# Kernel optimization log

Hardware: AMD Instinct MI355X
Metric: run time of the kernel (lower is better)

Reference implementation:

```python
import jax, jax.numpy as jnp
import numpy as np


def setup_inputs() -> dict:
    key = jax.random.key(0)
    ks = jax.random.split(key, 9)
    B, C, PF = 4, 256, 4096
    C8 = C // 8
    scale_qk = 1.0 / np.sqrt(C)
    return {
        "x": jax.random.normal(ks[0], (B, C, PF), dtype=jnp.float32),
        "xh1": jax.random.normal(ks[1], (B, C, PF), dtype=jnp.float32),
        "xl1": jax.random.normal(ks[2], (B, C, PF), dtype=jnp.float32),
        "Wq": jax.random.normal(ks[3], (C8, C), dtype=jnp.float32) * scale_qk,
        "bq": jnp.zeros((C8,), dtype=jnp.float32),
        "Wk": jax.random.normal(ks[4], (C8, C), dtype=jnp.float32) * scale_qk,
        "bk": jnp.zeros((C8,), dtype=jnp.float32),
        "Wv": jax.random.normal(ks[5], (C, C), dtype=jnp.float32) * scale_qk,
        "bv": jnp.zeros((C,), dtype=jnp.float32),
        "gamma1": jnp.array([0.5], dtype=jnp.float32),
        "gamma2": jnp.array([0.5], dtype=jnp.float32),
    }


def reference(x, xh1, xl1, Wq, bq, Wk, bk, Wv, bv, gamma1, gamma2):
    # x, xh1, xl1: (B, C, N) with N = H*W. Conv1x1 == channel-wise linear,
    # so the (B,C,H,W) reshape in the original is a no-op for the math.
    q = jnp.einsum("oc,bcn->bon", Wq, x) + bq[None, :, None]   # (B, C/8, N)
    k = jnp.einsum("oc,bcn->bon", Wk, x) + bk[None, :, None]   # (B, C/8, N)
    # energy[b, n, m] = q[:, :, n] . k[:, :, m]  (NO 1/sqrt(d) scale, as in source)
    energy = jnp.einsum("bcn,bcm->bnm", q, k)                  # (B, N, N)
    attention = jax.nn.softmax(energy, axis=-1)                # softmax over keys m
    vh = jnp.einsum("oc,bcn->bon", Wv, xh1) + bv[None, :, None]  # (B, C, N)
    vl = jnp.einsum("oc,bcn->bon", Wv, xl1) + bv[None, :, None]  # (B, C, N)
    # out = V @ attention^T : out[b, c, n] = sum_m vh[b, c, m] * attention[b, n, m]
    outh = jnp.einsum("bcm,bnm->bcn", vh, attention)
    outl = jnp.einsum("bcm,bnm->bcn", vl, attention)
    outh = xh1 * (gamma1 * outh)
    outl = xl1 * (gamma2 * outl)
    return outh, outl
```

## Files before the change

### kernel.cpp

```cpp
#include <hip/hip_runtime.h>
#include <math.h>

#define B_  4
#define C_  256
#define C8_ 32
#define N_  4096

typedef __attribute__((ext_vector_type(8))) short          bf16x8;
typedef __attribute__((ext_vector_type(8))) unsigned short us8;
typedef __attribute__((ext_vector_type(4))) float          f32x4;
typedef __attribute__((ext_vector_type(2))) float          f32x2;

__device__ inline unsigned short f2bf(float f) {
    unsigned u = __float_as_uint(f);
    u += 0x7FFFu + ((u >> 16) & 1u);
    return (unsigned short)(u >> 16);
}
__device__ inline unsigned pack2bf(float a, float b) {
    return (unsigned)f2bf(a) | ((unsigned)f2bf(b) << 16);
}

__global__ __launch_bounds__(256) void qk_proj_k(
    const float* __restrict__ x,  const float* __restrict__ Wq,
    const float* __restrict__ bq, const float* __restrict__ Wk,
    const float* __restrict__ bk, float* __restrict__ qt,
    float* __restrict__ ktt)
{
    __shared__ float Ws[64][36];
    __shared__ float Xs[32][132];
    const int b  = blockIdx.y;
    const int m0 = blockIdx.x * 128;
    const int t  = threadIdx.x;
    const int tx = t & 15;
    const int ty = t >> 4;
    const float* xb = x + (size_t)b * C_ * N_;

    float acc[4][8];
    #pragma unroll
    for (int i = 0; i < 4; ++i)
        #pragma unroll
        for (int j = 0; j < 8; ++j) acc[i][j] = 0.f;

    for (int k0 = 0; k0 < C_; k0 += 32) {
        __syncthreads();
        #pragma unroll
        for (int i = 0; i < 2; ++i) {
            int idx = t + i * 256, cc = idx >> 3, j = idx & 7;
            const float* src = (cc < 32 ? Wq + cc * C_ : Wk + (cc - 32) * C_) + k0 + j * 4;
            *(f32x4*)&Ws[cc][j * 4] = *(const f32x4*)src;
        }
        #pragma unroll
        for (int i = 0; i < 4; ++i) {
            int idx = t + i * 256, k = idx >> 5, j = idx & 31;
            *(f32x4*)&Xs[k][j * 4] = *(const f32x4*)(xb + (size_t)(k0 + k) * N_ + m0 + j * 4);
        }
        __syncthreads();
        for (int k = 0; k < 32; ++k) {
            float wv[4];
            #pragma unroll
            for (int i = 0; i < 4; ++i) wv[i] = Ws[ty * 4 + i][k];
            f32x4 x0 = *(const f32x4*)&Xs[k][tx * 8];
            f32x4 x1 = *(const f32x4*)&Xs[k][tx * 8 + 4];
            #pragma unroll
            for (int i = 0; i < 4; ++i) {
                acc[i][0] = fmaf(wv[i], x0[0], acc[i][0]);
                acc[i][1] = fmaf(wv[i], x0[1], acc[i][1]);
                acc[i][2] = fmaf(wv[i], x0[2], acc[i][2]);
                acc[i][3] = fmaf(wv[i], x0[3], acc[i][3]);
                acc[i][4] = fmaf(wv[i], x1[0], acc[i][4]);
                acc[i][5] = fmaf(wv[i], x1[1], acc[i][5]);
                acc[i][6] = fmaf(wv[i], x1[2], acc[i][6]);
                acc[i][7] = fmaf(wv[i], x1[3], acc[i][7]);
            }
        }
    }
    #pragma unroll
    for (int i = 0; i < 4; ++i) {
        const int cl = ty * 4 + i;
        if (cl < 32) {
            const float bqq = bq[cl];
            #pragma unroll
            for (int j = 0; j < 8; ++j)
                qt[((size_t)b * N_ + m0 + tx * 8 + j) * C8_ + cl] = acc[i][j] + bqq;
        } else {
            const float bkk = bk[cl - 32];
            f32x4 o0, o1;
            #pragma unroll
            for (int j = 0; j < 4; ++j) { o0[j] = acc[i][j] + bkk; o1[j] = acc[i][j + 4] + bkk; }
            float* dst = ktt + ((size_t)b * C8_ + cl - 32) * N_ + m0 + tx * 8;
            *(f32x4*)dst = o0;
            *(f32x4*)(dst + 4) = o1;
        }
    }
}

__global__ __launch_bounds__(256) void v_proj_k(
    const float* __restrict__ xh1, const float* __restrict__ xl1,
    const float* __restrict__ Wv,  const float* __restrict__ bv,
    unsigned short* __restrict__ vtc)
{
    __shared__ float Ws[64][36];
    __shared__ float Xs[32][132];
    const int b   = blockIdx.z & 3;
    const int s   = blockIdx.z >> 2;
    const int cc0 = blockIdx.y * 64;
    const int m0  = blockIdx.x * 128;
    const int t   = threadIdx.x;
    const int tx  = t & 15;
    const int ty  = t >> 4;
    const float* xb = (s ? xl1 : xh1) + (size_t)b * C_ * N_;

    float acc[4][8];
    #pragma unroll
    for (int i = 0; i < 4; ++i)
        #pragma unroll
        for (int j = 0; j < 8; ++j) acc[i][j] = 0.f;

    for (int k0 = 0; k0 < C_; k0 += 32) {
        __syncthreads();
        #pragma unroll
        for (int i = 0; i < 2; ++i) {
            int idx = t + i * 256, cc = idx >> 3, j = idx & 7;
            *(f32x4*)&Ws[cc][j * 4] = *(const f32x4*)(Wv + (size_t)(cc0 + cc) * C_ + k0 + j * 4);
        }
        #pragma unroll
        for (int i = 0; i < 4; ++i) {
            int idx = t + i * 256, k = idx >> 5, j = idx & 31;
            *(f32x4*)&Xs[k][j * 4] = *(const f32x4*)(xb + (size_t)(k0 + k) * N_ + m0 + j * 4);
        }
        __syncthreads();
        for (int k = 0; k < 32; ++k) {
            float wv[4];
            #pragma unroll
            for (int i = 0; i < 4; ++i) wv[i] = Ws[ty * 4 + i][k];
            f32x4 x0 = *(const f32x4*)&Xs[k][tx * 8];
            f32x4 x1 = *(const f32x4*)&Xs[k][tx * 8 + 4];
            #pragma unroll
            for (int i = 0; i < 4; ++i) {
                acc[i][0] = fmaf(wv[i], x0[0], acc[i][0]);
                acc[i][1] = fmaf(wv[i], x0[1], acc[i][1]);
                acc[i][2] = fmaf(wv[i], x0[2], acc[i][2]);
                acc[i][3] = fmaf(wv[i], x0[3], acc[i][3]);
                acc[i][4] = fmaf(wv[i], x1[0], acc[i][4]);
                acc[i][5] = fmaf(wv[i], x1[1], acc[i][5]);
                acc[i][6] = fmaf(wv[i], x1[2], acc[i][6]);
                acc[i][7] = fmaf(wv[i], x1[3], acc[i][7]);
            }
        }
    }
    #pragma unroll
    for (int i = 0; i < 4; ++i) {
        const int cc = cc0 + ty * 4 + i;
        const float bvv = bv[cc];
        us8 w;
        #pragma unroll
        for (int j = 0; j < 8; ++j) w[j] = f2bf(acc[i][j] + bvv);
        *(us8*)&vtc[((size_t)b * 512 + s * 256 + cc) * N_ + m0 + tx * 8] = w;
    }
}

__global__ __launch_bounds__(512, 4) void pv_k(
    const float* __restrict__ qt, const float* __restrict__ ktt,
    const unsigned short* __restrict__ vtc,
    const float* __restrict__ xh1, const float* __restrict__ xl1,
    const float* __restrict__ g1, const float* __restrict__ g2,
    float* __restrict__ out)
{
    __shared__ float          Kst[2][32][36];
    __shared__ unsigned short Ps[32][32];
    __shared__ unsigned short Vs[2][512][32];
    __shared__ float          Zrow[32];

    const int id   = blockIdx.x;
    const int b    = (id >> 1) & 3;
    const int nblk = ((id >> 3) << 1) | (id & 1);
    const int n0   = nblk * 32;

    const int t    = threadIdx.x;
    const int w    = t >> 6, lane = t & 63;
    const int lr   = lane & 15, ls = lane >> 4;
    const int wn   = w * 64;
    const int er   = t >> 4;
    const int eg   = t & 15;

    float q[32];
    {
        const float* qrow = qt + ((size_t)b * N_ + n0 + er) * C8_;
        #pragma unroll
        for (int c4 = 0; c4 < 8; ++c4) {
            f32x4 v = *(const f32x4*)(qrow + c4 * 4);
            q[c4*4+0] = v[0]; q[c4*4+1] = v[1]; q[c4*4+2] = v[2]; q[c4*4+3] = v[3];
        }
    }

    f32x4 acc[2][4];
    #pragma unroll
    for (int i = 0; i < 2; ++i)
        #pragma unroll
        for (int j = 0; j < 4; ++j) acc[i][j] = (f32x4){0.f, 0.f, 0.f, 0.f};
    float zpart = 0.f;

    const float*          kb   = ktt + (size_t)b * C8_ * N_;
    const unsigned short* vcol = vtc + (size_t)b * 512 * N_ + (size_t)t * N_;
    const int   kc   = t >> 3, kj = t & 7;
    const float* kptr = kb + (size_t)kc * N_ + kj * 4;
    const int   vsw  = (t >> 1) & 3;

    us8   vreg[4];
    f32x4 kreg;

    #pragma unroll
    for (int i = 0; i < 4; ++i) vreg[i] = *(const us8*)(vcol + i * 8);
    if (t < 256) kreg = *(const f32x4*)(kptr);
    #pragma unroll
    for (int i = 0; i < 4; ++i) *(us8*)&Vs[0][t][(i ^ vsw) * 8] = vreg[i];
    if (t < 256) *(f32x4*)&Kst[0][kc][kj * 4] = kreg;
    #pragma unroll
    for (int i = 0; i < 4; ++i) vreg[i] = *(const us8*)(vcol + 32 + i * 8);
    if (t < 256) kreg = *(const f32x4*)(kptr + 32);
    __syncthreads();

    int p = 0;
    for (int tile = 0; tile < N_ / 32; ++tile) {
        if (tile + 1 < N_ / 32) {
            #pragma unroll
            for (int i = 0; i < 4; ++i) *(us8*)&Vs[p ^ 1][t][(i ^ vsw) * 8] = vreg[i];
            if (t < 256) *(f32x4*)&Kst[p ^ 1][kc][kj * 4] = kreg;
        }
        if (tile + 2 < N_ / 32) {
            const int moff = (tile + 2) * 32;
            #pragma unroll
            for (int i = 0; i < 4; ++i) vreg[i] = *(const us8*)(vcol + moff + i * 8);
            if (t < 256) kreg = *(const f32x4*)(kptr + moff);
        }
        {
            float e0 = 0.f, e1 = 0.f;
            #pragma unroll
            for (int c = 0; c < 32; ++c) {
                f32x2 kv = *(const f32x2*)&Kst[p][c][eg * 2];
                e0 = fmaf(q[c], kv[0], e0);
                e1 = fmaf(q[c], kv[1], e1);
            }
            float p0 = __expf(e0 - 20.f);
            float p1 = __expf(e1 - 20.f);
            zpart += p0 + p1;
            *(unsigned*)&Ps[er][eg * 2] = pack2bf(p0, p1);
        }
        __syncthreads();
        {
            bf16x8 a0 = *(const bf16x8*)&Ps[lr][ls * 8];
            bf16x8 a1 = *(const bf16x8*)&Ps[16 + lr][ls * 8];
            #pragma unroll
            for (int fj = 0; fj < 4; ++fj) {
                const int col  = wn + fj * 16 + lr;
                const int slot = ls ^ ((col >> 1) & 3);
                bf16x8 bfr = *(const bf16x8*)&Vs[p][col][slot * 8];
                acc[0][fj] = __builtin_amdgcn_mfma_f32_16x16x32_bf16(a0, bfr, acc[0][fj], 0, 0, 0);
                acc[1][fj] = __builtin_amdgcn_mfma_f32_16x16x32_bf16(a1, bfr, acc[1][fj], 0, 0, 0);
            }
        }
        __syncthreads();
        p ^= 1;
    }

    #pragma unroll
    for (int m = 1; m < 16; m <<= 1) zpart += __shfl_xor(zpart, m, 16);
    if (eg == 0) Zrow[er] = zpart;
    __syncthreads();

    float rzf[2][4];
    #pragma unroll
    for (int fi = 0; fi < 2; ++fi)
        #pragma unroll
        for (int r = 0; r < 4; ++r) rzf[fi][r] = 1.f / Zrow[fi * 16 + ls * 4 + r];

    const float g1v = g1[0], g2v = g2[0];
    #pragma unroll
    for (int fi = 0; fi < 2; ++fi) {
        const int nb = fi * 16 + ls * 4;
        #pragma unroll
        for (int fj = 0; fj < 4; ++fj) {
            const int cc = wn + fj * 16 + lr;
            const int st = cc >> 8;
            const float  gv = st ? g2v : g1v;
            const float* xg = st ? xl1 : xh1;
            float* og = out + (st ? (size_t)B_ * C_ * N_ : (size_t)0);
            const size_t base = ((size_t)b * C_ + (cc & 255)) * N_ + n0 + nb;
            f32x4 xv = *(const f32x4*)(xg + base);
            f32x4 o;
            #pragma unroll
            for (int r = 0; r < 4; ++r)
                o[r] = xv[r] * (gv * (acc[fi][fj][r] * rzf[fi][r]));
            *(f32x4*)(og + base) = o;
        }
    }
}

extern "C" void kernel_launch(void* const* d_in, const int* in_sizes, int n_in,
                              void* d_out, int out_size, void* d_ws, size_t ws_size,
                              hipStream_t stream)
{
    const float* x   = (const float*)d_in[0];
    const float* xh1 = (const float*)d_in[1];
    const float* xl1 = (const float*)d_in[2];
    const float* Wq  = (const float*)d_in[3];
    const float* bq  = (const float*)d_in[4];
    const float* Wk  = (const float*)d_in[5];
    const float* bk  = (const float*)d_in[6];
    const float* Wv  = (const float*)d_in[7];
    const float* bv  = (const float*)d_in[8];
    const float* g1  = (const float*)d_in[9];
    const float* g2  = (const float*)d_in[10];
    float* out = (float*)d_out;

    char* pws = (char*)d_ws;
    float* qt  = (float*)pws;                 pws += (size_t)B_ * N_ * C8_ * 4;
    float* ktt = (float*)pws;                 pws += (size_t)B_ * N_ * C8_ * 4;
    unsigned short* vtc = (unsigned short*)pws;

    qk_proj_k<<<dim3(N_ / 128, B_),      256, 0, stream>>>(x, Wq, bq, Wk, bk, qt, ktt);
    v_proj_k <<<dim3(N_ / 128, 4, B_*2), 256, 0, stream>>>(xh1, xl1, Wv, bv, vtc);
    pv_k     <<<dim3((N_ / 32) * B_),    512, 0, stream>>>(qt, ktt, vtc,
                                                           xh1, xl1, g1, g2, out);
}
```

Before: 464.5 us.

## Use split-bf16 MFMA for projections and QK energy, stream V from registers

Replaces the FP32 FMA projection kernels with one templated kernel that splits inputs and weights into bf16 high/low parts and runs three MFMAs per product to approximate FP32 accuracy. In the attention kernel the scalar QK dot products move to split-bf16 MFMAs on half the waves while the other half stage K, and V fragments now load straight from global memory into registers, dropping the shared-memory V buffer. It also remaps blocks to group work by batch. This trades scalar FMA throughput for matrix-core throughput, at the cost of conversion overhead and a small precision loss.

```diff
diff --git a/kernel.cpp b/kernel.cpp
--- a/kernel.cpp
+++ b/kernel.cpp
@@ -5,157 +5,136 @@
 #define C_  256
 #define C8_ 32
 #define N_  4096
+#define NT_ 128
 
 typedef __attribute__((ext_vector_type(8))) short          bf16x8;
 typedef __attribute__((ext_vector_type(8))) unsigned short us8;
+typedef __attribute__((ext_vector_type(4))) unsigned short us4;
 typedef __attribute__((ext_vector_type(4))) float          f32x4;
-typedef __attribute__((ext_vector_type(2))) float          f32x2;
 
 __device__ inline unsigned short f2bf(float f) {
     unsigned u = __float_as_uint(f);
     u += 0x7FFFu + ((u >> 16) & 1u);
     return (unsigned short)(u >> 16);
 }
-__device__ inline unsigned pack2bf(float a, float b) {
-    return (unsigned)f2bf(a) | ((unsigned)f2bf(b) << 16);
-}
-
-__global__ __launch_bounds__(256) void qk_proj_k(
-    const float* __restrict__ x,  const float* __restrict__ Wq,
-    const float* __restrict__ bq, const float* __restrict__ Wk,
-    const float* __restrict__ bk, float* __restrict__ qt,
-    float* __restrict__ ktt)
+__device__ inline void splitbf(float v, unsigned short& h, unsigned short& l) {
+    unsigned short hh = f2bf(v);
+    float hf = __uint_as_float((unsigned)hh << 16);
+    h = hh; l = f2bf(v - hf);
+}
+__device__ inline bf16x8 asb(us8 v) { return __builtin_bit_cast(bf16x8, v); }
+
+template<int MODE>
+__global__ __launch_bounds__(256, 4) void proj_k(
+    const float* __restrict__ Xa, const float* __restrict__ Xb,
+    const float* __restrict__ Wa, const float* __restrict__ Wb,
+    const float* __restrict__ ba, const float* __restrict__ bb,
+    float* __restrict__ qt, float* __restrict__ ktt,
+    unsigned short* __restrict__ vtc)
 {
-    __shared__ float Ws[64][36];
-    __shared__ float Xs[32][132];
-    const int b  = blockIdx.y;
-    const int m0 = blockIdx.x * 128;
-    const int t  = threadIdx.x;
-    const int tx = t & 15;
-    const int ty = t >> 4;
-    const float* xb = x + (size_t)b * C_ * N_;
-
-    float acc[4][8];
+    __shared__ unsigned short XsH[32][66], XsL[32][66];
+    __shared__ unsigned short WsH[64][40], WsL[64][40];
+
+    const int m0 = blockIdx.x * 64;
+    int b, s, cc0;
+    const float* xptr;
+    if (MODE == 0) { b = blockIdx.z; s = 0; cc0 = 0;
+                     xptr = Xa + (size_t)b * C_ * N_; }
+    else           { b = blockIdx.z & 3; s = blockIdx.z >> 2; cc0 = blockIdx.y * 64;
+                     xptr = (s ? Xb : Xa) + (size_t)b * C_ * N_; }
+
+    const int t = threadIdx.x;
+    const int w = t >> 6, lane = t & 63, lr = lane & 15, ls = lane >> 4;
+
+    f32x4 acc[4];
     #pragma unroll
-    for (int i = 0; i < 4; ++i)
-        #pragma unroll
-        for (int j = 0; j < 8; ++j) acc[i][j] = 0.f;
+    for (int i = 0; i < 4; ++i) acc[i] = (f32x4){0.f, 0.f, 0.f, 0.f};
+
+    const int skk = t >> 3, smo = (t & 7) * 8;
+    const int scc = t >> 2, sko = (t & 3) * 8;
+    const float* wrow;
+    if (MODE == 0) wrow = (scc < 32) ? (Wa + (size_t)scc * C_) : (Wb + (size_t)(scc - 32) * C_);
+    else           wrow = Wa + (size_t)(cc0 + scc) * C_;
 
     for (int k0 = 0; k0 < C_; k0 += 32) {
         __syncthreads();
-        #pragma unroll
-        for (int i = 0; i < 2; ++i) {
-            int idx = t + i * 256, cc = idx >> 3, j = idx & 7;
-            const float* src = (cc < 32 ? Wq + cc * C_ : Wk + (cc - 32) * C_) + k0 + j * 4;
-            *(f32x4*)&Ws[cc][j * 4] = *(const f32x4*)src;
-        }
-        #pragma unroll
-        for (int i = 0; i < 4; ++i) {
-            int idx = t + i * 256, k = idx >> 5, j = idx & 31;
-            *(f32x4*)&Xs[k][j * 4] = *(const f32x4*)(xb + (size_t)(k0 + k) * N_ + m0 + j * 4);
+        {
+            const float* src = xptr + (size_t)(k0 + skk) * N_ + m0 + smo;
+            f32x4 a = *(const f32x4*)src, c = *(const f32x4*)(src + 4);
+            unsigned short h[8], l[8];
+            splitbf(a[0],h[0],l[0]); splitbf(a[1],h[1],l[1]);
+            splitbf(a[2],h[2],l[2]); splitbf(a[3],h[3],l[3]);
+            splitbf(c[0],h[4],l[4]); splitbf(c[1],h[5],l[5]);
+            splitbf(c[2],h[6],l[6]); splitbf(c[3],h[7],l[7]);
+            unsigned* dh = (unsigned*)&XsH[skk][smo];
+            unsigned* dl = (unsigned*)&XsL[skk][smo];
+            #pragma unroll
+            for (int i = 0; i < 4; ++i) {
+                dh[i] = (unsigned)h[2*i] | ((unsigned)h[2*i+1] << 16);
+                dl[i] = (unsigned)l[2*i] | ((unsigned)l[2*i+1] << 16);
+            }
+        }
+        {
+            f32x4 a = *(const f32x4*)(wrow + k0 + sko);
+            f32x4 c = *(const f32x4*)(wrow + k0 + sko + 4);
+            us8 h, l; unsigned short hh, ll;
+            splitbf(a[0],hh,ll); h[0]=hh; l[0]=ll;
+            splitbf(a[1],hh,ll); h[1]=hh; l[1]=ll;
+            splitbf(a[2],hh,ll); h[2]=hh; l[2]=ll;
+            splitbf(a[3],hh,ll); h[3]=hh; l[3]=ll;
+            splitbf(c[0],hh,ll); h[4]=hh; l[4]=ll;
+            splitbf(c[1],hh,ll); h[5]=hh; l[5]=ll;
+            splitbf(c[2],hh,ll); h[6]=hh; l[6]=ll;
+            splitbf(c[3],hh,ll); h[7]=hh; l[7]=ll;
+            *(us8*)&WsH[scc][sko] = h;
+            *(us8*)&WsL[scc][sko] = l;
         }
         __syncthreads();
-        for (int k = 0; k < 32; ++k) {
-            float wv[4];
-            #pragma unroll
-            for (int i = 0; i < 4; ++i) wv[i] = Ws[ty * 4 + i][k];
-            f32x4 x0 = *(const f32x4*)&Xs[k][tx * 8];
-            f32x4 x1 = *(const f32x4*)&Xs[k][tx * 8 + 4];
-            #pragma unroll
-            for (int i = 0; i < 4; ++i) {
-                acc[i][0] = fmaf(wv[i], x0[0], acc[i][0]);
-                acc[i][1] = fmaf(wv[i], x0[1], acc[i][1]);
-                acc[i][2] = fmaf(wv[i], x0[2], acc[i][2]);
-                acc[i][3] = fmaf(wv[i], x0[3], acc[i][3]);
-                acc[i][4] = fmaf(wv[i], x1[0], acc[i][4]);
-                acc[i][5] = fmaf(wv[i], x1[1], acc[i][5]);
-                acc[i][6] = fmaf(wv[i], x1[2], acc[i][6]);
-                acc[i][7] = fmaf(wv[i], x1[3], acc[i][7]);
+        us8 ahu, alu;
+        #pragma unroll
+        for (int j = 0; j < 8; ++j) {
+            ahu[j] = XsH[ls*8 + j][w*16 + lr];
+            alu[j] = XsL[ls*8 + j][w*16 + lr];
+        }
+        bf16x8 ah = asb(ahu), al = asb(alu);
+        #pragma unroll
+        for (int at = 0; at < 4; ++at) {
+            bf16x8 bh = asb(*(const us8*)&WsH[at*16 + lr][ls*8]);
+            bf16x8 bl = asb(*(const us8*)&WsL[at*16 + lr][ls*8]);
+            acc[at] = __builtin_amdgcn_mfma_f32_16x16x32_bf16(ah, bh, acc[at], 0, 0, 0);
+            acc[at] = __builtin_amdgcn_mfma_f32_16x16x32_bf16(ah, bl, acc[at], 0, 0, 0);
+            acc[at] = __builtin_amdgcn_mfma_f32_16x16x32_bf16(al, bh, acc[at], 0, 0, 0);
+        }
+    }
+
+    const int mrow = m0 + w*16 + ls*4;
+    if (MODE == 0) {
+        #pragma unroll
+        for (int at = 0; at < 4; ++at) {
+            const int cc = at*16 + lr;
+            if (at < 2) {
+                const float bia = ba[cc];
+                #pragma unroll
+                for (int r = 0; r < 4; ++r)
+                    qt[((size_t)b * N_ + mrow + r) * C8_ + cc] = acc[at][r] + bia;
+            } else {
+                const float bia = bb[cc - 32];
+                f32x4 o;
+                #pragma unroll
+                for (int r = 0; r < 4; ++r) o[r] = acc[at][r] + bia;
+                *(f32x4*)&ktt[((size_t)b * C8_ + cc - 32) * N_ + mrow] = o;
             }
         }
-    }
-    #pragma unroll
-    for (int i = 0; i < 4; ++i) {
-        const int cl = ty * 4 + i;
-        if (cl < 32) {
-            const float bqq = bq[cl];
-            #pragma unroll
-            for (int j = 0; j < 8; ++j)
-                qt[((size_t)b * N_ + m0 + tx * 8 + j) * C8_ + cl] = acc[i][j] + bqq;
-        } else {
-            const float bkk = bk[cl - 32];
-            f32x4 o0, o1;
-            #pragma unroll
-            for (int j = 0; j < 4; ++j) { o0[j] = acc[i][j] + bkk; o1[j] = acc[i][j + 4] + bkk; }
-            float* dst = ktt + ((size_t)b * C8_ + cl - 32) * N_ + m0 + tx * 8;
-            *(f32x4*)dst = o0;
-            *(f32x4*)(dst + 4) = o1;
-        }
-    }
-}
-
-__global__ __launch_bounds__(256) void v_proj_k(
-    const float* __restrict__ xh1, const float* __restrict__ xl1,
-    const float* __restrict__ Wv,  const float* __restrict__ bv,
-    unsigned short* __restrict__ vtc)
-{
-    __shared__ float Ws[64][36];
-    __shared__ float Xs[32][132];
-    const int b   = blockIdx.z & 3;
-    const int s   = blockIdx.z >> 2;
-    const int cc0 = blockIdx.y * 64;
-    const int m0  = blockIdx.x * 128;
-    const int t   = threadIdx.x;
-    const int tx  = t & 15;
-    const int ty  = t >> 4;
-    const float* xb = (s ? xl1 : xh1) + (size_t)b * C_ * N_;
-
-    float acc[4][8];
-    #pragma unroll
-    for (int i = 0; i < 4; ++i)
-        #pragma unroll
-        for (int j = 0; j < 8; ++j) acc[i][j] = 0.f;
-
-    for (int k0 = 0; k0 < C_; k0 += 32) {
-        __syncthreads();
-        #pragma unroll
-        for (int i = 0; i < 2; ++i) {
-            int idx = t + i * 256, cc = idx >> 3, j = idx & 7;
-            *(f32x4*)&Ws[cc][j * 4] = *(const f32x4*)(Wv + (size_t)(cc0 + cc) * C_ + k0 + j * 4);
-        }
-        #pragma unroll
-        for (int i = 0; i < 4; ++i) {
-            int idx = t + i * 256, k = idx >> 5, j = idx & 31;
-            *(f32x4*)&Xs[k][j * 4] = *(const f32x4*)(xb + (size_t)(k0 + k) * N_ + m0 + j * 4);
-        }
-        __syncthreads();
-        for (int k = 0; k < 32; ++k) {
-            float wv[4];
-            #pragma unroll
-            for (int i = 0; i < 4; ++i) wv[i] = Ws[ty * 4 + i][k];
-            f32x4 x0 = *(const f32x4*)&Xs[k][tx * 8];
-            f32x4 x1 = *(const f32x4*)&Xs[k][tx * 8 + 4];
-            #pragma unroll
-            for (int i = 0; i < 4; ++i) {
-                acc[i][0] = fmaf(wv[i], x0[0], acc[i][0]);
-                acc[i][1] = fmaf(wv[i], x0[1], acc[i][1]);
-                acc[i][2] = fmaf(wv[i], x0[2], acc[i][2]);
-                acc[i][3] = fmaf(wv[i], x0[3], acc[i][3]);
-                acc[i][4] = fmaf(wv[i], x1[0], acc[i][4]);
-                acc[i][5] = fmaf(wv[i], x1[1], acc[i][5]);
-                acc[i][6] = fmaf(wv[i], x1[2], acc[i][6]);
-                acc[i][7] = fmaf(wv[i], x1[3], acc[i][7]);
-            }
-        }
-    }
-    #pragma unroll
-    for (int i = 0; i < 4; ++i) {
-        const int cc = cc0 + ty * 4 + i;
-        const float bvv = bv[cc];
-        us8 w;
-        #pragma unroll
-        for (int j = 0; j < 8; ++j) w[j] = f2bf(acc[i][j] + bvv);
-        *(us8*)&vtc[((size_t)b * 512 + s * 256 + cc) * N_ + m0 + tx * 8] = w;
+    } else {
+        #pragma unroll
+        for (int at = 0; at < 4; ++at) {
+            const int cc = cc0 + at*16 + lr;
+            const float bia = ba[cc];
+            us4 o;
+            #pragma unroll
+            for (int r = 0; r < 4; ++r) o[r] = f2bf(acc[at][r] + bia);
+            *(us4*)&vtc[((size_t)b * 512 + s * 256 + cc) * N_ + mrow] = o;
+        }
     }
 }
 
@@ -166,31 +145,36 @@
     const float* __restrict__ g1, const float* __restrict__ g2,
     float* __restrict__ out)
 {
-    __shared__ float          Kst[2][32][36];
-    __shared__ unsigned short Ps[32][32];
-    __shared__ unsigned short Vs[2][512][32];
-    __shared__ float          Zrow[32];
-
-    const int id   = blockIdx.x;
-    const int b    = (id >> 1) & 3;
-    const int nblk = ((id >> 3) << 1) | (id & 1);
-    const int n0   = nblk * 32;
-
-    const int t    = threadIdx.x;
-    const int w    = t >> 6, lane = t & 63;
-    const int lr   = lane & 15, ls = lane >> 4;
-    const int wn   = w * 64;
-    const int er   = t >> 4;
-    const int eg   = t & 15;
-
-    float q[32];
-    {
-        const float* qrow = qt + ((size_t)b * N_ + n0 + er) * C8_;
-        #pragma unroll
-        for (int c4 = 0; c4 < 8; ++c4) {
-            f32x4 v = *(const f32x4*)(qrow + c4 * 4);
-            q[c4*4+0] = v[0]; q[c4*4+1] = v[1]; q[c4*4+2] = v[2]; q[c4*4+3] = v[3];
-        }
+    __shared__ unsigned short KsH[2][32][34];
+    __shared__ unsigned short KsL[2][32][34];
+    __shared__ unsigned short Ps[32][40];
+    __shared__ float          Zpart[2][32];
+
+    const int orig = blockIdx.x;
+    const int wg   = (orig & 7) * 64 + (orig >> 3);
+    const int b    = wg >> 7;
+    const int n0   = (wg & 127) * 32;
+
+    const int t = threadIdx.x, w = t >> 6, lane = t & 63;
+    const int lr = lane & 15, ls = lane >> 4;
+    const int wn = w * 64;
+    const bool ew = (w < 4);
+    const int rt = (w >> 1) & 1, mt = w & 1;
+
+    bf16x8 qh = {}, ql = {};
+    if (ew) {
+        const float* qrow = qt + ((size_t)b * N_ + n0 + rt*16 + lr) * C8_ + ls*8;
+        f32x4 q0 = *(const f32x4*)qrow, q1 = *(const f32x4*)(qrow + 4);
+        us8 hu, lu; unsigned short hh, ll;
+        splitbf(q0[0],hh,ll); hu[0]=hh; lu[0]=ll;
+        splitbf(q0[1],hh,ll); hu[1]=hh; lu[1]=ll;
+        splitbf(q0[2],hh,ll); hu[2]=hh; lu[2]=ll;
+        splitbf(q0[3],hh,ll); hu[3]=hh; lu[3]=ll;
+        splitbf(q1[0],hh,ll); hu[4]=hh; lu[4]=ll;
+        splitbf(q1[1],hh,ll); hu[5]=hh; lu[5]=ll;
+        splitbf(q1[2],hh,ll); hu[6]=hh; lu[6]=ll;
+        splitbf(q1[3],hh,ll); hu[7]=hh; lu[7]=ll;
+        qh = asb(hu); ql = asb(lu);
     }
 
     f32x4 acc[2][4];
@@ -198,89 +182,124 @@
     for (int i = 0; i < 2; ++i)
         #pragma unroll
         for (int j = 0; j < 4; ++j) acc[i][j] = (f32x4){0.f, 0.f, 0.f, 0.f};
-    float zpart = 0.f;
-
-    const float*          kb   = ktt + (size_t)b * C8_ * N_;
-    const unsigned short* vcol = vtc + (size_t)b * 512 * N_ + (size_t)t * N_;
-    const int   kc   = t >> 3, kj = t & 7;
-    const float* kptr = kb + (size_t)kc * N_ + kj * 4;
-    const int   vsw  = (t >> 1) & 3;
-
-    us8   vreg[4];
-    f32x4 kreg;
-
-    #pragma unroll
-    for (int i = 0; i < 4; ++i) vreg[i] = *(const us8*)(vcol + i * 8);
-    if (t < 256) kreg = *(const f32x4*)(kptr);
-    #pragma unroll
-    for (int i = 0; i < 4; ++i) *(us8*)&Vs[0][t][(i ^ vsw) * 8] = vreg[i];
-    if (t < 256) *(f32x4*)&Kst[0][kc][kj * 4] = kreg;
-    #pragma unroll
-    for (int i = 0; i < 4; ++i) vreg[i] = *(const us8*)(vcol + 32 + i * 8);
-    if (t < 256) kreg = *(const f32x4*)(kptr + 32);
+    float zreg[4] = {0.f, 0.f, 0.f, 0.f};
+
+    const unsigned short* vbase = vtc + (size_t)b * 512 * N_;
+    const unsigned short* vp0 = vbase + (size_t)(wn +  0 + lr) * N_ + ls*8;
+    const unsigned short* vp1 = vbase + (size_t)(wn + 16 + lr) * N_ + ls*8;
+    const unsigned short* vp2 = vbase + (size_t)(wn + 32 + lr) * N_ + ls*8;
+    const unsigned short* vp3 = vbase + (size_t)(wn + 48 + lr) * N_ + ls*8;
+
+    const int ts = t - 256, kc = (ts & 255) >> 3, kmq = (ts & 7) * 4;
+    const float* kptr = ktt + ((size_t)b * C8_ + kc) * N_ + kmq;
+
+    us8 vA0, vA1, vA2, vA3, vB0, vB1, vB2, vB3;
+
+    if (!ew) {
+        f32x4 kv = *(const f32x4*)kptr;
+        unsigned short h0,h1,h2,h3,l0,l1,l2,l3;
+        splitbf(kv[0],h0,l0); splitbf(kv[1],h1,l1);
+        splitbf(kv[2],h2,l2); splitbf(kv[3],h3,l3);
+        unsigned* dh = (unsigned*)&KsH[0][kc][kmq];
+        unsigned* dl = (unsigned*)&KsL[0][kc][kmq];
+        dh[0] = (unsigned)h0 | ((unsigned)h1 << 16);
+        dh[1] = (unsigned)h2 | ((unsigned)h3 << 16);
+        dl[0] = (unsigned)l0 | ((unsigned)l1 << 16);
+        dl[1] = (unsigned)l2 | ((unsigned)l3 << 16);
+    }
+    vA0 = *(const us8*)vp0; vA1 = *(const us8*)vp1;
+    vA2 = *(const us8*)vp2; vA3 = *(const us8*)vp3;
     __syncthreads();
 
-    int p = 0;
-    for (int tile = 0; tile < N_ / 32; ++tile) {
-        if (tile + 1 < N_ / 32) {
-            #pragma unroll
-            for (int i = 0; i < 4; ++i) *(us8*)&Vs[p ^ 1][t][(i ^ vsw) * 8] = vreg[i];
-            if (t < 256) *(f32x4*)&Kst[p ^ 1][kc][kj * 4] = kreg;
-        }
-        if (tile + 2 < N_ / 32) {
-            const int moff = (tile + 2) * 32;
-            #pragma unroll
-            for (int i = 0; i < 4; ++i) vreg[i] = *(const us8*)(vcol + moff + i * 8);
-            if (t < 256) kreg = *(const f32x4*)(kptr + moff);
-        }
-        {
-            float e0 = 0.f, e1 = 0.f;
-            #pragma unroll
-            for (int c = 0; c < 32; ++c) {
-                f32x2 kv = *(const f32x2*)&Kst[p][c][eg * 2];
-                e0 = fmaf(q[c], kv[0], e0);
-                e1 = fmaf(q[c], kv[1], e1);
+    auto body = [&](int CUR, int NXT, us8& VC0, us8& VC1, us8& VC2, us8& VC3,
+                    us8& VN0, us8& VN1, us8& VN2, us8& VN3, int TILE) {
+        const int tn = TILE + 1;
+        f32x4 kreg;
+        if (tn < NT_) {
+            VN0 = *(const us8*)(vp0 + tn*32);
+            VN1 = *(const us8*)(vp1 + tn*32);
+            VN2 = *(const us8*)(vp2 + tn*32);
+            VN3 = *(const us8*)(vp3 + tn*32);
+            if (!ew) kreg = *(const f32x4*)(kptr + tn*32);
+        }
+        if (ew) {
+            us8 khu, klu;
+            #pragma unroll
+            for (int j = 0; j < 8; ++j) {
+                khu[j] = KsH[CUR][ls*8 + j][mt*16 + lr];
+                klu[j] = KsL[CUR][ls*8 + j][mt*16 + lr];
             }
-            float p0 = __expf(e0 - 20.f);
-            float p1 = __expf(e1 - 20.f);
-            zpart += p0 + p1;
-            *(unsigned*)&Ps[er][eg * 2] = pack2bf(p0, p1);
+            bf16x8 kh = asb(khu), kl = asb(klu);
+            f32x4 ea = (f32x4){0.f, 0.f, 0.f, 0.f};
+            ea = __builtin_amdgcn_mfma_f32_16x16x32_bf16(qh, kh, ea, 0, 0, 0);
+            ea = __builtin_amdgcn_mfma_f32_16x16x32_bf16(qh, kl, ea, 0, 0, 0);
+            ea = __builtin_amdgcn_mfma_f32_16x16x32_bf16(ql, kh, ea, 0, 0, 0);
+            #pragma unroll
+            for (int r = 0; r < 4; ++r) {
+                float pe = __expf(ea[r] - 20.f);
+                zreg[r] += pe;
+                Ps[rt*16 + ls*4 + r][mt*16 + lr] = f2bf(pe);
+            }
         }
         __syncthreads();
         {
-            bf16x8 a0 = *(const bf16x8*)&Ps[lr][ls * 8];
-            bf16x8 a1 = *(const bf16x8*)&Ps[16 + lr][ls * 8];
-            #pragma unroll
-            for (int fj = 0; fj < 4; ++fj) {
-                const int col  = wn + fj * 16 + lr;
-                const int slot = ls ^ ((col >> 1) & 3);
-                bf16x8 bfr = *(const bf16x8*)&Vs[p][col][slot * 8];
-                acc[0][fj] = __builtin_amdgcn_mfma_f32_16x16x32_bf16(a0, bfr, acc[0][fj], 0, 0, 0);
-                acc[1][fj] = __builtin_amdgcn_mfma_f32_16x16x32_bf16(a1, bfr, acc[1][fj], 0, 0, 0);
-            }
+            bf16x8 pa0 = asb(*(const us8*)&Ps[lr][ls*8]);
+            bf16x8 pa1 = asb(*(const us8*)&Ps[16 + lr][ls*8]);
+            bf16x8 v0 = asb(VC0), v1 = asb(VC1), v2 = asb(VC2), v3 = asb(VC3);
+            acc[0][0] = __builtin_amdgcn_mfma_f32_16x16x32_bf16(pa0, v0, acc[0][0], 0,0,0);
+            acc[1][0] = __builtin_amdgcn_mfma_f32_16x16x32_bf16(pa1, v0, acc[1][0], 0,0,0);
+            acc[0][1] = __builtin_amdgcn_mfma_f32_16x16x32_bf16(pa0, v1, acc[0][1], 0,0,0);
+            acc[1][1] = __builtin_amdgcn_mfma_f32_16x16x32_bf16(pa1, v1, acc[1][1], 0,0,0);
+            acc[0][2] = __builtin_amdgcn_mfma_f32_16x16x32_bf16(pa0, v2, acc[0][2], 0,0,0);
+            acc[1][2] = __builtin_amdgcn_mfma_f32_16x16x32_bf16(pa1, v2, acc[1][2], 0,0,0);
+            acc[0][3] = __builtin_amdgcn_mfma_f32_16x16x32_bf16(pa0, v3, acc[0][3], 0,0,0);
+            acc[1][3] = __builtin_amdgcn_mfma_f32_16x16x32_bf16(pa1, v3, acc[1][3], 0,0,0);
+        }
+        if (tn < NT_ && !ew) {
+            unsigned short h0,h1,h2,h3,l0,l1,l2,l3;
+            splitbf(kreg[0],h0,l0); splitbf(kreg[1],h1,l1);
+            splitbf(kreg[2],h2,l2); splitbf(kreg[3],h3,l3);
+            unsigned* dh = (unsigned*)&KsH[NXT][kc][kmq];
+            unsigned* dl = (unsigned*)&KsL[NXT][kc][kmq];
+            dh[0] = (unsigned)h0 | ((unsigned)h1 << 16);
+            dh[1] = (unsigned)h2 | ((unsigned)h3 << 16);
+            dl[0] = (unsigned)l0 | ((unsigned)l1 << 16);
+            dl[1] = (unsigned)l2 | ((unsigned)l3 << 16);
         }
         __syncthreads();
-        p ^= 1;
-    }
-
-    #pragma unroll
-    for (int m = 1; m < 16; m <<= 1) zpart += __shfl_xor(zpart, m, 16);
-    if (eg == 0) Zrow[er] = zpart;
+    };
+
+    for (int tile = 0; tile < NT_; tile += 2) {
+        body(0, 1, vA0, vA1, vA2, vA3, vB0, vB1, vB2, vB3, tile);
+        body(1, 0, vB0, vB1, vB2, vB3, vA0, vA1, vA2, vA3, tile + 1);
+    }
+
+    if (ew) {
+        #pragma unroll
+        for (int r = 0; r < 4; ++r) {
+            float z = zreg[r];
+            z += __shfl_xor(z, 1, 16); z += __shfl_xor(z, 2, 16);
+            z += __shfl_xor(z, 4, 16); z += __shfl_xor(z, 8, 16);
+            if (lr == 0) Zpart[mt][rt*16 + ls*4 + r] = z;
+        }
+    }
     __syncthreads();
 
     float rzf[2][4];
     #pragma unroll
     for (int fi = 0; fi < 2; ++fi)
         #pragma unroll
-        for (int r = 0; r < 4; ++r) rzf[fi][r] = 1.f / Zrow[fi * 16 + ls * 4 + r];
-
+        for (int r = 0; r < 4; ++r) {
+            const int row = fi*16 + ls*4 + r;
+            rzf[fi][r] = 1.f / (Zpart[0][row] + Zpart[1][row]);
+        }
     const float g1v = g1[0], g2v = g2[0];
     #pragma unroll
     for (int fi = 0; fi < 2; ++fi) {
-        const int nb = fi * 16 + ls * 4;
+        const int nb = fi*16 + ls*4;
         #pragma unroll
         for (int fj = 0; fj < 4; ++fj) {
-            const int cc = wn + fj * 16 + lr;
+            const int cc = wn + fj*16 + lr;
             const int st = cc >> 8;
             const float  gv = st ? g2v : g1v;
             const float* xg = st ? xl1 : xh1;
@@ -318,8 +337,9 @@
     float* ktt = (float*)pws;                 pws += (size_t)B_ * N_ * C8_ * 4;
     unsigned short* vtc = (unsigned short*)pws;
 
-    qk_proj_k<<<dim3(N_ / 128, B_),      256, 0, stream>>>(x, Wq, bq, Wk, bk, qt, ktt);
-    v_proj_k <<<dim3(N_ / 128, 4, B_*2), 256, 0, stream>>>(xh1, xl1, Wv, bv, vtc);
-    pv_k     <<<dim3((N_ / 32) * B_),    512, 0, stream>>>(qt, ktt, vtc,
-                                                           xh1, xl1, g1, g2, out);
-}
+    proj_k<0><<<dim3(N_ / 64, 1, B_),     256, 0, stream>>>(
+        x, nullptr, Wq, Wk, bq, bk, qt, ktt, nullptr);
+    proj_k<1><<<dim3(N_ / 64, 4, B_ * 2), 256, 0, stream>>>(
+        xh1, xl1, Wv, nullptr, bv, nullptr, nullptr, nullptr, vtc);
+    pv_k<<<dim3(512), 512, 0, stream>>>(qt, ktt, vtc, xh1, xl1, g1, g2, out);
+}
```

Result: faster. 388.7 us (-16.3%).
